# Kernel optimization log

Hardware: AMD Instinct MI355X
Metric: run time of the kernel (lower is better)

Reference implementation:

```python
import jax, jax.numpy as jnp
import numpy as np

B, S, HID = 2, 2048, 1024
NH, DK, DV = 4, 256, 256   # head_k_dim = head_v_dim = 1024 / 4
KSZ = 4                    # conv_size
EPS = 1e-5


def causal_conv1d(x, w):
    # x: [B, S, C] channels-last, w: [C, K] depthwise kernel (torch [C,1,K] squeezed)
    K = w.shape[1]
    Sn = x.shape[1]
    xp = jnp.pad(x, ((0, 0), (K - 1, 0), (0, 0)))
    # cross-correlation with left padding K-1 -> causal: out[t] = sum_j w[:,j] * x[t-(K-1)+j]
    out = xp[:, 0:Sn, :] * w[:, 0]
    for j in range(1, K):
        out = out + xp[:, j:j + Sn, :] * w[:, j]
    return out


def l2norm(x, eps=1e-6):
    return x * jax.lax.rsqrt(jnp.sum(x * x, axis=-1, keepdims=True) + eps)


def rms_norm(x, w, eps=EPS):
    return x * jax.lax.rsqrt(jnp.mean(x * x, axis=-1, keepdims=True) + eps) * w


def delta_rule(q, k, v, beta):
    # q,k: [B,S,H,dk]; v: [B,S,H,dv]; beta: [B,S,H]
    Bn, Sn, Hn, dk = q.shape
    dv = v.shape[-1]
    N = Bn * Hn
    qs = jnp.moveaxis(q, 1, 0).reshape(Sn, N, dk)
    ks = jnp.moveaxis(k, 1, 0).reshape(Sn, N, dk)
    vs = jnp.moveaxis(v, 1, 0).reshape(Sn, N, dv)
    bs = jnp.moveaxis(beta, 1, 0).reshape(Sn, N)

    S0 = jnp.zeros((N, dk, dv), q.dtype)

    def step(St, inp):
        qt, kt, vt, bt = inp
        kS = jnp.einsum('nk,nkv->nv', kt, St)              # k^T S
        St = St + jnp.einsum('nk,nv->nkv', kt, bt[:, None] * (vt - kS))
        ot = jnp.einsum('nk,nkv->nv', qt, St)
        return St, ot

    _, o = jax.lax.scan(step, S0, (qs, ks, vs, bs))        # o: [S, N, dv]
    o = o.reshape(Sn, Bn, Hn, dv)
    return jnp.moveaxis(o, 0, 1)                            # [B,S,H,dv]


def setup_inputs() -> dict:
    key = jax.random.key(0)
    ks = jax.random.split(key, 10)
    w_scale = 2.0 ** (-2.5) * np.sqrt(6.0 / (HID + HID))   # xavier_uniform with gain 2^-2.5
    u = lambda k, shp, s: jax.random.uniform(k, shp, jnp.float32, -s, s)
    return {
        'hidden_states': jax.random.normal(ks[0], (B, S, HID), jnp.float32),
        'Wq': u(ks[1], (HID, NH * DK), w_scale),
        'Wk': u(ks[2], (HID, NH * DK), w_scale),
        'Wv': u(ks[3], (HID, NH * DV), w_scale),
        'Wb': u(ks[4], (HID, NH), w_scale),
        'conv_q': jax.random.normal(ks[5], (NH * DK, KSZ), jnp.float32) * 0.2,
        'conv_k': jax.random.normal(ks[6], (NH * DK, KSZ), jnp.float32) * 0.2,
        'conv_v': jax.random.normal(ks[7], (NH * DV, KSZ), jnp.float32) * 0.2,
        'norm_w': jnp.ones((DV,), jnp.float32),
        'Wo': u(ks[8], (NH * DV, HID), w_scale),
    }


def reference(hidden_states, Wq, Wk, Wv, Wb, conv_q, conv_k, conv_v, norm_w, Wo):
    q = hidden_states @ Wq                                  # [B,S,key_dim]
    k = hidden_states @ Wk
    v = hidden_states @ Wv
    q = causal_conv1d(q, conv_q)
    k = causal_conv1d(k, conv_k)
    v = causal_conv1d(v, conv_v)
    q = jax.nn.silu(q).reshape(B, S, NH, DK)
    k = jax.nn.silu(k).reshape(B, S, NH, DK)
    v = jax.nn.silu(v).reshape(B, S, NH, DV)
    beta = jax.nn.sigmoid(hidden_states @ Wb)               # [B,S,H]
    q = l2norm(q)
    k = l2norm(k)
    o = delta_rule(q, k, v, beta)                           # [B,S,H,dv]
    o = rms_norm(o, norm_w)
    o = o.reshape(B, S, NH * DV) @ Wo                       # [B,S,HID]
    return o
```

## Files before the change

kernel.cpp:

```cpp
#include <hip/hip_runtime.h>
#include <math.h>

#define BB   2
#define SS   2048
#define HIDD 1024
#define ROWS 4096
#define NCH  32
#define CH   64

typedef unsigned short u16t;
typedef unsigned int   u32t;

typedef __attribute__((ext_vector_type(8))) short bf16x8;
typedef __attribute__((ext_vector_type(4))) float f32x4;

__device__ __forceinline__ float bf2f(u16t u) { return __uint_as_float(((u32t)u) << 16); }
__device__ __forceinline__ u16t f2bf(float f) {
    u32t b = __float_as_uint(f);
    return (u16t)((b + 0x7FFFu + ((b >> 16) & 1u)) >> 16);
}
__device__ __forceinline__ float lo_bf(u32t u) { return __uint_as_float(u << 16); }
__device__ __forceinline__ float hi_bf(u32t u) { return __uint_as_float(u & 0xFFFF0000u); }

__device__ __forceinline__ float waveReduceSum(float v) {
#pragma unroll
    for (int m = 1; m < 64; m <<= 1) v += __shfl_xor(v, m, 64);
    return v;
}

__device__ __forceinline__ void gload16(const void* g, void* l) {
    __builtin_amdgcn_global_load_lds(
        (const __attribute__((address_space(1))) unsigned int*)g,
        (__attribute__((address_space(3))) unsigned int*)l, 16, 0, 0);
}

#define MFMA(a, b, c) __builtin_amdgcn_mfma_f32_16x16x32_bf16(a, b, c, 0, 0, 0)

__global__ __launch_bounds__(256) void f2bf_kernel(const float* __restrict__ in,
                                                   u16t* __restrict__ out) {
    const size_t idx = ((size_t)blockIdx.x * 256 + threadIdx.x) * 8;
    float4 a = *(const float4*)&in[idx];
    float4 b = *(const float4*)&in[idx + 4];
    ushort4 o1, o2;
    o1.x = f2bf(a.x); o1.y = f2bf(a.y); o1.z = f2bf(a.z); o1.w = f2bf(a.w);
    o2.x = f2bf(b.x); o2.y = f2bf(b.y); o2.z = f2bf(b.z); o2.w = f2bf(b.w);
    *(ushort4*)&out[idx] = o1;
    *(ushort4*)&out[idx + 4] = o2;
}

__global__ __launch_bounds__(256) void transpose_w4(const float* __restrict__ W0,
                                                    const float* __restrict__ W1,
                                                    const float* __restrict__ W2,
                                                    const float* __restrict__ W3,
                                                    u16t* __restrict__ T0,
                                                    u16t* __restrict__ T1,
                                                    u16t* __restrict__ T2,
                                                    u16t* __restrict__ T3) {
    __shared__ u16t tile[64][65];
    const int z = blockIdx.z;
    const float* W = (z == 0) ? W0 : (z == 1) ? W1 : (z == 2) ? W2 : W3;
    u16t* WT = (z == 0) ? T0 : (z == 1) ? T1 : (z == 2) ? T2 : T3;
    const int t = threadIdx.x;
    const int r0 = blockIdx.y * 64, c0 = blockIdx.x * 64;
    const int lr = t >> 2, lc4 = (t & 3) * 16;
#pragma unroll
    for (int m = 0; m < 4; ++m) {
        float4 v = *(const float4*)&W[(size_t)(r0 + lr) * 1024 + c0 + lc4 + m * 4];
        tile[lr][lc4 + m * 4 + 0] = f2bf(v.x);
        tile[lr][lc4 + m * 4 + 1] = f2bf(v.y);
        tile[lr][lc4 + m * 4 + 2] = f2bf(v.z);
        tile[lr][lc4 + m * 4 + 3] = f2bf(v.w);
    }
    __syncthreads();
#pragma unroll
    for (int m = 0; m < 16; ++m)
        WT[(size_t)(c0 + lr) * 1024 + r0 + lc4 + m] = tile[lc4 + m][lr];
}

__global__ __launch_bounds__(256) void gemm_mfma(const u16t* __restrict__ A,
                                                 const u16t* __restrict__ BT,
                                                 float* __restrict__ Cf,
                                                 u16t* __restrict__ Cb, int obf,
                                                 int M, int N, int K,
                                                 size_t bStrideP, size_t cStrideP,
                                                 int CX) {
    __shared__ u16t As[128 * 64];
    __shared__ u16t Bs[128 * 64];
    const int t = threadIdx.x, l = t & 63, w = t >> 6;
    const int wr = w >> 1, wc = w & 1;

    const int lin = blockIdx.y * gridDim.x + blockIdx.x;
    const int xcd = lin & 7, idx = lin >> 3;
    const int Wc = gridDim.x / CX;
    const int Hc = (gridDim.y * CX) >> 3;
    const int colB = (xcd % CX) * Wc + idx % Wc;
    const int rowB = (xcd / CX) * Hc + idx / Wc;

    const int rowBase = rowB * 128, colBase = colB * 128;
    const int l15 = l & 15, g4 = l >> 4;

    const int bplane = colBase >> 10;
    const int bcol = colBase & 1023;

    const int srow = l >> 3;
    const int sj = (l & 7) ^ srow;
    const u16t* aSrc = A + (size_t)(rowBase + srow) * K + sj * 8;
    const u16t* bSrc = BT + (size_t)bplane * bStrideP + (size_t)(bcol + srow) * K + sj * 8;

    f32x4 acc[4][4];
#pragma unroll
    for (int i = 0; i < 4; ++i)
#pragma unroll
        for (int j = 0; j < 4; ++j) acc[i][j] = (f32x4){0.f, 0.f, 0.f, 0.f};

    for (int k0 = 0; k0 < K; k0 += 64) {
#pragma unroll
        for (int i = 0; i < 4; ++i) {
            const int rb = (i * 4 + w) * 8;
            gload16(aSrc + (size_t)rb * K + k0, &As[rb * 64]);
            gload16(bSrc + (size_t)rb * K + k0, &Bs[rb * 64]);
        }
        __syncthreads();
#pragma unroll
        for (int kh = 0; kh < 2; ++kh) {
            bf16x8 aF[4], bF[4];
#pragma unroll
            for (int mi = 0; mi < 4; ++mi) {
                const int row = wr * 64 + mi * 16 + l15;
                const int phys = (kh * 4 + g4) ^ (row & 7);
                aF[mi] = *(const bf16x8*)&As[row * 64 + phys * 8];
            }
#pragma unroll
            for (int ni = 0; ni < 4; ++ni) {
                const int row = wc * 64 + ni * 16 + l15;
                const int phys = (kh * 4 + g4) ^ (row & 7);
                bF[ni] = *(const bf16x8*)&Bs[row * 64 + phys * 8];
            }
#pragma unroll
            for (int mi = 0; mi < 4; ++mi)
#pragma unroll
                for (int ni = 0; ni < 4; ++ni)
                    acc[mi][ni] = MFMA(aF[mi], bF[ni], acc[mi][ni]);
        }
        __syncthreads();
    }
#pragma unroll
    for (int mi = 0; mi < 4; ++mi)
#pragma unroll
        for (int ni = 0; ni < 4; ++ni)
#pragma unroll
            for (int rg = 0; rg < 4; ++rg) {
                const int row = rowBase + wr * 64 + mi * 16 + g4 * 4 + rg;
                const int col = colBase + wc * 64 + ni * 16 + l15;
                const int plane = col >> 10, cc = col & 1023;
                const float v = acc[mi][ni][rg];
                if (obf) Cb[(size_t)plane * cStrideP + (size_t)row * 1024 + cc] = f2bf(v);
                else     Cf[(size_t)plane * cStrideP + (size_t)row * 1024 + cc] = v;
            }
}

__global__ __launch_bounds__(256) void beta_kernel(const float* __restrict__ X,
                                                   const float* __restrict__ Wb,
                                                   float* __restrict__ beta) {
    const int gw   = (blockIdx.x * blockDim.x + threadIdx.x) >> 6;
    const int lane = threadIdx.x & 63;
    if (gw >= ROWS) return;
    const float* x = X + (size_t)gw * HIDD;
    float a0 = 0.f, a1 = 0.f, a2 = 0.f, a3 = 0.f;
#pragma unroll
    for (int i = 0; i < 4; ++i) {
        const int k = lane * 16 + i * 4;
        float4 xv = *(const float4*)&x[k];
        float4 w0 = *(const float4*)&Wb[(size_t)(k + 0) * 4];
        float4 w1 = *(const float4*)&Wb[(size_t)(k + 1) * 4];
        float4 w2 = *(const float4*)&Wb[(size_t)(k + 2) * 4];
        float4 w3 = *(const float4*)&Wb[(size_t)(k + 3) * 4];
        a0 += xv.x * w0.x + xv.y * w1.x + xv.z * w2.x + xv.w * w3.x;
        a1 += xv.x * w0.y + xv.y * w1.y + xv.z * w2.y + xv.w * w3.y;
        a2 += xv.x * w0.z + xv.y * w1.z + xv.z * w2.z + xv.w * w3.z;
        a3 += xv.x * w0.w + xv.y * w1.w + xv.z * w2.w + xv.w * w3.w;
    }
    a0 = waveReduceSum(a0); a1 = waveReduceSum(a1);
    a2 = waveReduceSum(a2); a3 = waveReduceSum(a3);
    if (lane == 0) {
        float4 o = make_float4(1.f / (1.f + expf(-a0)), 1.f / (1.f + expf(-a1)),
                               1.f / (1.f + expf(-a2)), 1.f / (1.f + expf(-a3)));
        *(float4*)&beta[(size_t)gw * 4] = o;
    }
}

__global__ __launch_bounds__(256) void conv_qv(const u16t* __restrict__ inQ,
                                               const float* __restrict__ wQ,
                                               u16t* __restrict__ outQ,
                                               const u16t* __restrict__ inV,
                                               const float* __restrict__ wV,
                                               u16t* __restrict__ outV) {
    const int isQ = (blockIdx.y == 0);
    const u16t* in = isQ ? inQ : inV;
    const float* w = isQ ? wQ : wV;
    u16t* out      = isQ ? outQ : outV;
    const int doL2 = isQ;

    const int gw   = (blockIdx.x * blockDim.x + threadIdx.x) >> 6;
    const int lane = threadIdx.x & 63;
    const int r = gw >> 2;
    const int h = gw & 3;
    const int b = r >> 11;
    const int s = r & 2047;
    const int c4 = h * 256 + lane * 4;

    const float4 wr0 = *(const float4*)&w[(size_t)(c4 + 0) * 4];
    const float4 wr1 = *(const float4*)&w[(size_t)(c4 + 1) * 4];
    const float4 wr2 = *(const float4*)&w[(size_t)(c4 + 2) * 4];
    const float4 wr3 = *(const float4*)&w[(size_t)(c4 + 3) * 4];

    const size_t rowB = (size_t)(b << 11);
    float x0[4] = {0, 0, 0, 0}, x1[4] = {0, 0, 0, 0}, x2[4] = {0, 0, 0, 0}, x3[4];
    ushort4 u;
    if (s >= 3) { u = *(const ushort4*)&in[(rowB + s - 3) * HIDD + c4];
        x0[0] = bf2f(u.x); x0[1] = bf2f(u.y); x0[2] = bf2f(u.z); x0[3] = bf2f(u.w); }
    if (s >= 2) { u = *(const ushort4*)&in[(rowB + s - 2) * HIDD + c4];
        x1[0] = bf2f(u.x); x1[1] = bf2f(u.y); x1[2] = bf2f(u.z); x1[3] = bf2f(u.w); }
    if (s >= 1) { u = *(const ushort4*)&in[(rowB + s - 1) * HIDD + c4];
        x2[0] = bf2f(u.x); x2[1] = bf2f(u.y); x2[2] = bf2f(u.z); x2[3] = bf2f(u.w); }
    u = *(const ushort4*)&in[(rowB + s) * HIDD + c4];
    x3[0] = bf2f(u.x); x3[1] = bf2f(u.y); x3[2] = bf2f(u.z); x3[3] = bf2f(u.w);

    float y0 = wr0.x * x0[0] + wr0.y * x1[0] + wr0.z * x2[0] + wr0.w * x3[0];
    float y1 = wr1.x * x0[1] + wr1.y * x1[1] + wr1.z * x2[1] + wr1.w * x3[1];
    float y2 = wr2.x * x0[2] + wr2.y * x1[2] + wr2.z * x2[2] + wr2.w * x3[2];
    float y3 = wr3.x * x0[3] + wr3.y * x1[3] + wr3.z * x2[3] + wr3.w * x3[3];

    y0 = y0 / (1.f + expf(-y0)); y1 = y1 / (1.f + expf(-y1));
    y2 = y2 / (1.f + expf(-y2)); y3 = y3 / (1.f + expf(-y3));

    if (doL2) {
        float ss = y0 * y0 + y1 * y1 + y2 * y2 + y3 * y3;
        ss = waveReduceSum(ss);
        float sc = rsqrtf(ss + 1e-6f);
        y0 *= sc; y1 *= sc; y2 *= sc; y3 *= sc;
    }
    ushort4 o;
    o.x = f2bf(y0); o.y = f2bf(y1); o.z = f2bf(y2); o.w = f2bf(y3);
    *(ushort4*)&out[(size_t)r * HIDD + c4] = o;
}

__global__ __launch_bounds__(256) void conv_k_chunk(const u16t* __restrict__ pre,
                                                    const float* __restrict__ w,
                                                    u16t* __restrict__ rowout,
                                                    u16t* __restrict__ trout) {
    const int t = threadIdx.x;
    const int bh = blockIdx.x >> 5, c = blockIdx.x & 31;
    const int b = bh >> 2, h = bh & 3;
    const int i = t >> 2, g = t & 3;
    const int s = c * 64 + i;
    const size_t row = (size_t)b * 2048 + s;
    const int ch0 = h * 256 + g * 64;
    const int cloc = g * 64;
    float y[64];
#pragma unroll
    for (int m = 0; m < 8; ++m) {
        const int cm = ch0 + m * 8;
        uint4 x3 = *(const uint4*)&pre[row * 1024 + cm];
        uint4 x2 = (s >= 1) ? *(const uint4*)&pre[(row - 1) * 1024 + cm] : make_uint4(0, 0, 0, 0);
        uint4 x1 = (s >= 2) ? *(const uint4*)&pre[(row - 2) * 1024 + cm] : make_uint4(0, 0, 0, 0);
        uint4 x0 = (s >= 3) ? *(const uint4*)&pre[(row - 3) * 1024 + cm] : make_uint4(0, 0, 0, 0);
        u32t c0[4] = {x0.x, x0.y, x0.z, x0.w};
        u32t c1[4] = {x1.x, x1.y, x1.z, x1.w};
        u32t c2[4] = {x2.x, x2.y, x2.z, x2.w};
        u32t c3[4] = {x3.x, x3.y, x3.z, x3.w};
#pragma unroll
        for (int p = 0; p < 4; ++p) {
            const int ch = m * 8 + p * 2;
            float4 wA = *(const float4*)&w[(size_t)(ch0 + ch) * 4];
            float4 wB = *(const float4*)&w[(size_t)(ch0 + ch + 1) * 4];
            float ya = wA.x * lo_bf(c0[p]) + wA.y * lo_bf(c1[p]) + wA.z * lo_bf(c2[p]) + wA.w * lo_bf(c3[p]);
            float yb = wB.x * hi_bf(c0[p]) + wB.y * hi_bf(c1[p]) + wB.z * hi_bf(c2[p]) + wB.w * hi_bf(c3[p]);
            ya = ya / (1.f + expf(-ya));
            yb = yb / (1.f + expf(-yb));
            y[ch] = ya; y[ch + 1] = yb;
        }
    }
    float ss = 0.f;
#pragma unroll
    for (int e = 0; e < 64; ++e) ss += y[e] * y[e];
    ss += __shfl_xor(ss, 1);
    ss += __shfl_xor(ss, 2);
    const float sc = rsqrtf(ss + 1e-6f);
#pragma unroll
    for (int m = 0; m < 8; ++m) {
        uint4 o;
        u32t* op = (u32t*)&o;
#pragma unroll
        for (int p = 0; p < 4; ++p) {
            u16t a = f2bf(y[m * 8 + p * 2] * sc);
            u16t bb2 = f2bf(y[m * 8 + p * 2 + 1] * sc);
            op[p] = (u32t)a | ((u32t)bb2 << 16);
        }
        *(uint4*)&rowout[row * 1024 + ch0 + m * 8] = o;
    }
#pragma unroll
    for (int e = 0; e < 64; ++e)
        trout[((size_t)bh * 256 + cloc + e) * 2048 + s] = f2bf(y[e] * sc);
}

__global__ __launch_bounds__(256) void prep_kernel(const u16t* __restrict__ qcb,
                                                   const u16t* __restrict__ kcb,
                                                   const float* __restrict__ beta,
                                                   u16t* __restrict__ Tghi,
                                                   u16t* __restrict__ Tglo,
                                                   u16t* __restrict__ Agb) {
    __shared__ float KT[256][68];
    __shared__ float QT[256][68];
    __shared__ float Af[64][68];
    const int t = threadIdx.x;
    const int bhc = blockIdx.x;
    const int bh = bhc >> 5, c = bhc & 31;
    const int b = bh >> 2, h = bh & 3;
    const int tb = b * SS + c * CH;

    {
        const int i = t & 63, rb = t >> 6;
        const u16t* kg = kcb + (size_t)(tb + i) * HIDD + h * 256 + rb * 64;
        const u16t* qg = qcb + (size_t)(tb + i) * HIDD + h * 256 + rb * 64;
#pragma unroll
        for (int m = 0; m < 8; ++m) {
            uint4 kv = ((const uint4*)kg)[m];
            uint4 qv = ((const uint4*)qg)[m];
            u32t kw[4] = {kv.x, kv.y, kv.z, kv.w};
            u32t qw[4] = {qv.x, qv.y, qv.z, qv.w};
#pragma unroll
            for (int n = 0; n < 4; ++n) {
                int rr = rb * 64 + m * 8 + n * 2;
                KT[rr][i]     = lo_bf(kw[n]);
                KT[rr + 1][i] = hi_bf(kw[n]);
                QT[rr][i]     = lo_bf(qw[n]);
                QT[rr + 1][i] = hi_bf(qw[n]);
            }
        }
    }
    __syncthreads();

    const int it = t & 63, jb = t >> 6;
    float kk[16], qk[16];
#pragma unroll
    for (int m = 0; m < 16; ++m) { kk[m] = 0.f; qk[m] = 0.f; }
#pragma unroll 2
    for (int r = 0; r < 256; ++r) {
        float ki = KT[r][it];
        float qi = QT[r][it];
        float4 ka = *(const float4*)&KT[r][jb * 16 + 0];
        float4 kb = *(const float4*)&KT[r][jb * 16 + 4];
        float4 kc = *(const float4*)&KT[r][jb * 16 + 8];
        float4 kd = *(const float4*)&KT[r][jb * 16 + 12];
        float kj[16] = {ka.x, ka.y, ka.z, ka.w, kb.x, kb.y, kb.z, kb.w,
                        kc.x, kc.y, kc.z, kc.w, kd.x, kd.y, kd.z, kd.w};
#pragma unroll
        for (int m = 0; m < 16; ++m) { kk[m] += ki * kj[m]; qk[m] += qi * kj[m]; }
    }

    const float bta = beta[(size_t)(tb + it) * 4 + h];
    u16t* ag = Agb + (size_t)bhc * 4096 + (size_t)it * 64 + jb * 16;
#pragma unroll
    for (int m = 0; m < 16; ++m) {
        int j = jb * 16 + m;
        Af[it][j] = (j < it) ? bta * kk[m] : 0.f;
    }
#pragma unroll
    for (int m4 = 0; m4 < 4; ++m4) {
        ushort4 o;
        o.x = f2bf((jb * 16 + m4 * 4 + 0 <= it) ? qk[m4 * 4 + 0] : 0.f);
        o.y = f2bf((jb * 16 + m4 * 4 + 1 <= it) ? qk[m4 * 4 + 1] : 0.f);
        o.z = f2bf((jb * 16 + m4 * 4 + 2 <= it) ? qk[m4 * 4 + 2] : 0.f);
        o.w = f2bf((jb * 16 + m4 * 4 + 3 <= it) ? qk[m4 * 4 + 3] : 0.f);
        *(ushort4*)&ag[m4 * 4] = o;
    }
    __syncthreads();

    if (t < 64) {
        const int ccol = t;
        float tc[64];
#pragma unroll
        for (int j = 0; j < 64; ++j) tc[j] = (j == ccol) ? 1.f : 0.f;
#pragma unroll
        for (int i = 1; i < 64; ++i) {
            float a = 0.f;
#pragma unroll
            for (int j = 0; j < i; ++j) a += Af[i][j] * tc[j];
            tc[i] -= a;
        }
        u16t* th = Tghi + (size_t)bhc * 4096;
        u16t* tl = Tglo + (size_t)bhc * 4096;
#pragma unroll
        for (int i = 0; i < 64; ++i) {
            u16t hi = f2bf(tc[i]);
            th[i * 64 + ccol] = hi;
            tl[i * 64 + ccol] = f2bf(tc[i] - bf2f(hi));
        }
    }
}

__global__ __launch_bounds__(256, 1) void scan_mfma(const u16t* __restrict__ qcb,
                                                    const u16t* __restrict__ kcb,
                                                    const u16t* __restrict__ ktr,
                                                    const u16t* __restrict__ vcb,
                                                    const float* __restrict__ beta,
                                                    const u16t* __restrict__ TghiG,
                                                    const u16t* __restrict__ TgloG,
                                                    const u16t* __restrict__ AgbG,
                                                    u16t* __restrict__ o_raw) {
    __shared__ u16t Shi[16 * 256];
    __shared__ u16t Slo[16 * 256];
    __shared__ u16t Rhi[16 * 64];
    __shared__ u16t Rlo[16 * 64];
    __shared__ u16t Uhi[16 * 64];
    __shared__ u16t Ulo[16 * 64];

    const int t = threadIdx.x, l = t & 63, w = t >> 6;
    const int bh = blockIdx.x & 7, vt = blockIdx.x >> 3;
    const int b = bh >> 2, h = bh & 3;
    const int vcol0 = vt * 16;
    const int vlow = l & 15, g4 = l >> 4;

    for (int i = t; i < 16 * 256; i += 256) { Shi[i] = 0; Slo[i] = 0; }
    f32x4 sf[4];
#pragma unroll
    for (int q = 0; q < 4; ++q) sf[q] = (f32x4){0.f, 0.f, 0.f, 0.f};

    bf16x8 kf[8], qf[8], tfh[2], tfl[2], af[2], kcf[8];
    u16t vfb[4];
    float bta[4];

    auto loadKQ = [&](int c) {
        const size_t rb = (size_t)(b * 2048 + c * 64 + 16 * w + vlow) * 1024 + h * 256 + g4 * 8;
#pragma unroll
        for (int ks = 0; ks < 8; ++ks) {
            kf[ks] = *(const bf16x8*)(kcb + rb + ks * 32);
            qf[ks] = *(const bf16x8*)(qcb + rb + ks * 32);
        }
    };
    auto loadVB = [&](int c) {
        const int r0 = b * 2048 + c * 64 + 16 * w + 4 * g4;
#pragma unroll
        for (int rg = 0; rg < 4; ++rg) {
            vfb[rg] = vcb[(size_t)(r0 + rg) * 1024 + h * 256 + vcol0 + vlow];
            bta[rg] = beta[(size_t)(r0 + rg) * 4 + h];
        }
    };
    auto loadT = [&](int c) {
        const size_t tb2 = (size_t)(bh * 32 + c) * 4096 + (size_t)(16 * w + vlow) * 64 + g4 * 8;
        tfh[0] = *(const bf16x8*)(TghiG + tb2);
        tfh[1] = *(const bf16x8*)(TghiG + tb2 + 32);
        tfl[0] = *(const bf16x8*)(TgloG + tb2);
        tfl[1] = *(const bf16x8*)(TgloG + tb2 + 32);
    };
    auto loadA = [&](int c) {
        const size_t tb2 = (size_t)(bh * 32 + c) * 4096 + (size_t)(16 * w + vlow) * 64 + g4 * 8;
        af[0] = *(const bf16x8*)(AgbG + tb2);
        af[1] = *(const bf16x8*)(AgbG + tb2 + 32);
    };
    auto loadKC = [&](int c) {
        const size_t cb2 = ((size_t)bh * 256 + 64 * w + vlow) * 2048 + c * 64 + g4 * 8;
#pragma unroll
        for (int q2 = 0; q2 < 4; ++q2) {
            kcf[q2 * 2 + 0] = *(const bf16x8*)(ktr + cb2 + (size_t)(16 * q2) * 2048);
            kcf[q2 * 2 + 1] = *(const bf16x8*)(ktr + cb2 + (size_t)(16 * q2) * 2048 + 32);
        }
    };

    loadKQ(0); loadVB(0); loadT(0); loadA(0); loadKC(0);
    __syncthreads();

    for (int c = 0; c < NCH; ++c) {
        const int cn = (c + 1 < NCH) ? c + 1 : c;
        const int trow0 = b * 2048 + c * 64;

        f32x4 Wacc = (f32x4){0.f, 0.f, 0.f, 0.f};
        f32x4 O1   = (f32x4){0.f, 0.f, 0.f, 0.f};
#pragma unroll
        for (int ks = 0; ks < 8; ++ks) {
            const int pb = (((ks * 4 + g4) ^ (vlow & 7)) << 3);
            bf16x8 bH = *(const bf16x8*)&Shi[vlow * 256 + pb];
            bf16x8 bL = *(const bf16x8*)&Slo[vlow * 256 + pb];
            Wacc = MFMA(kf[ks], bH, Wacc); Wacc = MFMA(kf[ks], bL, Wacc);
            O1   = MFMA(qf[ks], bH, O1);   O1   = MFMA(qf[ks], bL, O1);
        }
        {
            const int tslot = 2 * w + (g4 >> 1);
            const int base = vlow * 64 + ((tslot ^ (vlow & 7)) << 3) + ((g4 & 1) << 2);
            u16t rh[4], rl[4];
#pragma unroll
            for (int rg = 0; rg < 4; ++rg) {
                float rv = bta[rg] * (bf2f(vfb[rg]) - Wacc[rg]);
                rh[rg] = f2bf(rv);
                rl[rg] = f2bf(rv - bf2f(rh[rg]));
            }
            uint2 ph, pl;
            ph.x = (u32t)rh[0] | ((u32t)rh[1] << 16); ph.y = (u32t)rh[2] | ((u32t)rh[3] << 16);
            pl.x = (u32t)rl[0] | ((u32t)rl[1] << 16); pl.y = (u32t)rl[2] | ((u32t)rl[3] << 16);
            *(uint2*)&Rhi[base] = ph;
            *(uint2*)&Rlo[base] = pl;
        }
        loadKQ(cn);
        loadVB(cn);
        __syncthreads();

        f32x4 Uacc = (f32x4){0.f, 0.f, 0.f, 0.f};
#pragma unroll
        for (int ks = 0; ks < 2; ++ks) {
            const int pb = (((ks * 4 + g4) ^ (vlow & 7)) << 3);
            bf16x8 bH = *(const bf16x8*)&Rhi[vlow * 64 + pb];
            bf16x8 bL = *(const bf16x8*)&Rlo[vlow * 64 + pb];
            Uacc = MFMA(tfh[ks], bH, Uacc);
            Uacc = MFMA(tfh[ks], bL, Uacc);
            Uacc = MFMA(tfl[ks], bH, Uacc);
        }
        {
            const int tslot = 2 * w + (g4 >> 1);
            const int base = vlow * 64 + ((tslot ^ (vlow & 7)) << 3) + ((g4 & 1) << 2);
            u16t uh[4], ul[4];
#pragma unroll
            for (int rg = 0; rg < 4; ++rg) {
                uh[rg] = f2bf(Uacc[rg]);
                ul[rg] = f2bf(Uacc[rg] - bf2f(uh[rg]));
            }
            uint2 ph, pl;
            ph.x = (u32t)uh[0] | ((u32t)uh[1] << 16); ph.y = (u32t)uh[2] | ((u32t)uh[3] << 16);
            pl.x = (u32t)ul[0] | ((u32t)ul[1] << 16); pl.y = (u32t)ul[2] | ((u32t)ul[3] << 16);
            *(uint2*)&Uhi[base] = ph;
            *(uint2*)&Ulo[base] = pl;
        }
        loadT(cn);
        __syncthreads();

        bf16x8 uhf[2], ulf[2];
#pragma unroll
        for (int ks = 0; ks < 2; ++ks) {
            const int pb = (((ks * 4 + g4) ^ (vlow & 7)) << 3);
            uhf[ks] = *(const bf16x8*)&Uhi[vlow * 64 + pb];
            ulf[ks] = *(const bf16x8*)&Ulo[vlow * 64 + pb];
        }
        f32x4 Oacc = O1;
#pragma unroll
        for (int ks = 0; ks < 2; ++ks) {
            Oacc = MFMA(af[ks], uhf[ks], Oacc);
            Oacc = MFMA(af[ks], ulf[ks], Oacc);
        }
#pragma unroll
        for (int rg = 0; rg < 4; ++rg)
            o_raw[(size_t)(trow0 + 16 * w + 4 * g4 + rg) * 1024 + h * 256 + vcol0 + vlow] = f2bf(Oacc[rg]);
        loadA(cn);

#pragma unroll
        for (int q = 0; q < 4; ++q) {
#pragma unroll
            for (int ks = 0; ks < 2; ++ks) {
                sf[q] = MFMA(kcf[q * 2 + ks], uhf[ks], sf[q]);
                sf[q] = MFMA(kcf[q * 2 + ks], ulf[ks], sf[q]);
            }
        }
        loadKC(cn);

#pragma unroll
        for (int q = 0; q < 4; ++q) {
            u16t sh[4], sl[4];
#pragma unroll
            for (int rg = 0; rg < 4; ++rg) {
                u16t hi = f2bf(sf[q][rg]);
                sh[rg] = hi;
                sl[rg] = f2bf(sf[q][rg] - bf2f(hi));
            }
            const int rslot = 8 * w + 2 * q + (g4 >> 1);
            const int base = vlow * 256 + ((rslot ^ (vlow & 7)) << 3) + ((g4 & 1) << 2);
            uint2 ph, pl;
            ph.x = (u32t)sh[0] | ((u32t)sh[1] << 16); ph.y = (u32t)sh[2] | ((u32t)sh[3] << 16);
            pl.x = (u32t)sl[0] | ((u32t)sl[1] << 16); pl.y = (u32t)sl[2] | ((u32t)sl[3] << 16);
            *(uint2*)&Shi[base] = ph;
            *(uint2*)&Slo[base] = pl;
        }
        __syncthreads();
    }
}

__global__ __launch_bounds__(256) void rms_kernel(const u16t* __restrict__ in,
                                                  const float* __restrict__ w,
                                                  u16t* __restrict__ out) {
    const int gw   = (blockIdx.x * blockDim.x + threadIdx.x) >> 6;
    const int lane = threadIdx.x & 63;
    const int r = gw >> 2;
    const int h = gw & 3;
    const size_t base = (size_t)r * HIDD + h * 256 + lane * 4;
    ushort4 xv = *(const ushort4*)&in[base];
    float x0 = bf2f(xv.x), x1 = bf2f(xv.y), x2 = bf2f(xv.z), x3 = bf2f(xv.w);
    float ss = x0 * x0 + x1 * x1 + x2 * x2 + x3 * x3;
    ss = waveReduceSum(ss);
    const float sc = rsqrtf(ss * (1.0f / 256.0f) + 1e-5f);
    float4 wv = *(const float4*)&w[lane * 4];
    ushort4 o;
    o.x = f2bf(x0 * sc * wv.x); o.y = f2bf(x1 * sc * wv.y);
    o.z = f2bf(x2 * sc * wv.z); o.w = f2bf(x3 * sc * wv.w);
    *(ushort4*)&out[base] = o;
}

extern "C" void kernel_launch(void* const* d_in, const int* in_sizes, int n_in,
                              void* d_out, int out_size, void* d_ws, size_t ws_size,
                              hipStream_t stream) {
    const float* X      = (const float*)d_in[0];
    const float* Wq     = (const float*)d_in[1];
    const float* Wk     = (const float*)d_in[2];
    const float* Wv     = (const float*)d_in[3];
    const float* Wb     = (const float*)d_in[4];
    const float* conv_q = (const float*)d_in[5];
    const float* conv_k = (const float*)d_in[6];
    const float* conv_v = (const float*)d_in[7];
    const float* norm_w = (const float*)d_in[8];
    const float* Wo     = (const float*)d_in[9];
    float* out = (float*)d_out;

    char* W8 = (char*)d_ws;
    const size_t MB = 1u << 20;
    u16t* Xbf   = (u16t*)(W8 + 0 * MB);
    u16t* o_raw = Xbf;
    u16t* qpre  = (u16t*)(W8 + 8 * MB);
    u16t* o_nrm = qpre;
    u16t* kpre  = (u16t*)(W8 + 16 * MB);
    u16t* Tghi  = (u16t*)(W8 + 16 * MB);
    u16t* Tglo  = (u16t*)(W8 + 18 * MB);
    u16t* Agb   = (u16t*)(W8 + 20 * MB);
    u16t* vpre  = (u16t*)(W8 + 24 * MB);
    u16t* ktr   = (u16t*)(W8 + 24 * MB);
    u16t* WqT   = (u16t*)(W8 + 32 * MB);
    u16t* qcb   = (u16t*)(W8 + 32 * MB);
    u16t* WkT   = (u16t*)(W8 + 40 * MB);
    u16t* kcb   = (u16t*)(W8 + 40 * MB);
    u16t* WvT   = (u16t*)(W8 + 48 * MB);
    u16t* vcb   = (u16t*)(W8 + 48 * MB);
    u16t* WoT   = (u16t*)(W8 + 56 * MB);
    float* betab = (float*)(W8 + 58 * MB);

    const size_t PL = 4194304;

    f2bf_kernel<<<2048, 256, 0, stream>>>(X, Xbf);
    transpose_w4<<<dim3(16, 16, 4), 256, 0, stream>>>(Wq, Wk, Wv, Wo, WqT, WkT, WvT, WoT);

    gemm_mfma<<<dim3(24, 32), 256, 0, stream>>>(Xbf, WqT, nullptr, qpre, 1,
                                                ROWS, 3072, HIDD, PL, PL, 2);
    beta_kernel<<<ROWS / 4, 256, 0, stream>>>(X, Wb, betab);

    conv_qv<<<dim3(ROWS, 2), 256, 0, stream>>>(qpre, conv_q, qcb, vpre, conv_v, vcb);
    conv_k_chunk<<<256, 256, 0, stream>>>(kpre, conv_k, kcb, ktr);

    prep_kernel<<<256, 256, 0, stream>>>(qcb, kcb, betab, Tghi, Tglo, Agb);
    scan_mfma<<<128, 256, 0, stream>>>(qcb, kcb, ktr, vcb, betab, Tghi, Tglo, Agb, o_raw);

    rms_kernel<<<ROWS, 256, 0, stream>>>(o_raw, norm_w, o_nrm);
    gemm_mfma<<<dim3(8, 32), 256, 0, stream>>>(o_nrm, WoT, out, nullptr, 0,
                                               ROWS, HIDD, HIDD, 0, 0, 1);
}
```

Before: 285.9 us.

## Process four value-column tiles per scan block to reuse K/Q/T/A fragments

Each scan block now handles 64 value columns (four 16-wide tiles) instead of 16, so the per-chunk K, Q, T, A and transposed-K fragments loaded from global memory are reused across four state slices. The grid shrinks from 128 to 32 blocks, and shared memory and accumulator registers grow fourfold. The goal is to cut redundant global loads of the shared operands, at the cost of parallelism (only 32 CUs busy on a chip with many more) and higher register pressure.

```diff
diff --git a/kernel.cpp b/kernel.cpp
--- a/kernel.cpp
+++ b/kernel.cpp
@@ -409,26 +409,29 @@
                                                     const u16t* __restrict__ TgloG,
                                                     const u16t* __restrict__ AgbG,
                                                     u16t* __restrict__ o_raw) {
-    __shared__ u16t Shi[16 * 256];
-    __shared__ u16t Slo[16 * 256];
-    __shared__ u16t Rhi[16 * 64];
-    __shared__ u16t Rlo[16 * 64];
-    __shared__ u16t Uhi[16 * 64];
-    __shared__ u16t Ulo[16 * 64];
+    __shared__ u16t Shi[4][16 * 256];
+    __shared__ u16t Slo[4][16 * 256];
+    __shared__ u16t Rhi[4][16 * 64];
+    __shared__ u16t Rlo[4][16 * 64];
+    __shared__ u16t Uhi[4][16 * 64];
+    __shared__ u16t Ulo[4][16 * 64];
 
     const int t = threadIdx.x, l = t & 63, w = t >> 6;
-    const int bh = blockIdx.x & 7, vt = blockIdx.x >> 3;
+    const int bh = blockIdx.x & 7, vq = blockIdx.x >> 3;
     const int b = bh >> 2, h = bh & 3;
-    const int vcol0 = vt * 16;
+    const int vbase = vq * 64;
     const int vlow = l & 15, g4 = l >> 4;
 
-    for (int i = t; i < 16 * 256; i += 256) { Shi[i] = 0; Slo[i] = 0; }
-    f32x4 sf[4];
-#pragma unroll
-    for (int q = 0; q < 4; ++q) sf[q] = (f32x4){0.f, 0.f, 0.f, 0.f};
+    for (int i = t; i < 4 * 16 * 256; i += 256) { (&Shi[0][0])[i] = 0; (&Slo[0][0])[i] = 0; }
+
+    f32x4 sf[4][4];
+#pragma unroll
+    for (int p = 0; p < 4; ++p)
+#pragma unroll
+        for (int q = 0; q < 4; ++q) sf[p][q] = (f32x4){0.f, 0.f, 0.f, 0.f};
 
     bf16x8 kf[8], qf[8], tfh[2], tfl[2], af[2], kcf[8];
-    u16t vfb[4];
+    u16t vfb[4][4];
     float bta[4];
 
     auto loadKQ = [&](int c) {
@@ -443,8 +446,10 @@
         const int r0 = b * 2048 + c * 64 + 16 * w + 4 * g4;
 #pragma unroll
         for (int rg = 0; rg < 4; ++rg) {
-            vfb[rg] = vcb[(size_t)(r0 + rg) * 1024 + h * 256 + vcol0 + vlow];
             bta[rg] = beta[(size_t)(r0 + rg) * 4 + h];
+#pragma unroll
+            for (int p = 0; p < 4; ++p)
+                vfb[p][rg] = vcb[(size_t)(r0 + rg) * 1024 + h * 256 + vbase + p * 16 + vlow];
         }
     };
     auto loadT = [&](int c) {
@@ -471,113 +476,125 @@
     loadKQ(0); loadVB(0); loadT(0); loadA(0); loadKC(0);
     __syncthreads();
 
+    const int tslot = 2 * w + (g4 >> 1);
+    const int rubase = vlow * 64 + ((tslot ^ (vlow & 7)) << 3) + ((g4 & 1) << 2);
+
     for (int c = 0; c < NCH; ++c) {
         const int cn = (c + 1 < NCH) ? c + 1 : c;
         const int trow0 = b * 2048 + c * 64;
 
-        f32x4 Wacc = (f32x4){0.f, 0.f, 0.f, 0.f};
-        f32x4 O1   = (f32x4){0.f, 0.f, 0.f, 0.f};
+        f32x4 Wacc[4], O1[4];
+#pragma unroll
+        for (int p = 0; p < 4; ++p) { Wacc[p] = (f32x4){0,0,0,0}; O1[p] = (f32x4){0,0,0,0}; }
 #pragma unroll
         for (int ks = 0; ks < 8; ++ks) {
             const int pb = (((ks * 4 + g4) ^ (vlow & 7)) << 3);
-            bf16x8 bH = *(const bf16x8*)&Shi[vlow * 256 + pb];
-            bf16x8 bL = *(const bf16x8*)&Slo[vlow * 256 + pb];
-            Wacc = MFMA(kf[ks], bH, Wacc); Wacc = MFMA(kf[ks], bL, Wacc);
-            O1   = MFMA(qf[ks], bH, O1);   O1   = MFMA(qf[ks], bL, O1);
-        }
-        {
-            const int tslot = 2 * w + (g4 >> 1);
-            const int base = vlow * 64 + ((tslot ^ (vlow & 7)) << 3) + ((g4 & 1) << 2);
+#pragma unroll
+            for (int p = 0; p < 4; ++p) {
+                bf16x8 bH = *(const bf16x8*)&Shi[p][vlow * 256 + pb];
+                bf16x8 bL = *(const bf16x8*)&Slo[p][vlow * 256 + pb];
+                Wacc[p] = MFMA(kf[ks], bH, Wacc[p]); Wacc[p] = MFMA(kf[ks], bL, Wacc[p]);
+                O1[p]   = MFMA(qf[ks], bH, O1[p]);   O1[p]   = MFMA(qf[ks], bL, O1[p]);
+            }
+        }
+#pragma unroll
+        for (int p = 0; p < 4; ++p) {
             u16t rh[4], rl[4];
 #pragma unroll
             for (int rg = 0; rg < 4; ++rg) {
-                float rv = bta[rg] * (bf2f(vfb[rg]) - Wacc[rg]);
+                float rv = bta[rg] * (bf2f(vfb[p][rg]) - Wacc[p][rg]);
                 rh[rg] = f2bf(rv);
                 rl[rg] = f2bf(rv - bf2f(rh[rg]));
             }
             uint2 ph, pl;
             ph.x = (u32t)rh[0] | ((u32t)rh[1] << 16); ph.y = (u32t)rh[2] | ((u32t)rh[3] << 16);
             pl.x = (u32t)rl[0] | ((u32t)rl[1] << 16); pl.y = (u32t)rl[2] | ((u32t)rl[3] << 16);
-            *(uint2*)&Rhi[base] = ph;
-            *(uint2*)&Rlo[base] = pl;
+            *(uint2*)&Rhi[p][rubase] = ph;
+            *(uint2*)&Rlo[p][rubase] = pl;
         }
         loadKQ(cn);
         loadVB(cn);
         __syncthreads();
 
-        f32x4 Uacc = (f32x4){0.f, 0.f, 0.f, 0.f};
+        f32x4 Uacc[4];
+#pragma unroll
+        for (int p = 0; p < 4; ++p) Uacc[p] = (f32x4){0,0,0,0};
 #pragma unroll
         for (int ks = 0; ks < 2; ++ks) {
             const int pb = (((ks * 4 + g4) ^ (vlow & 7)) << 3);
-            bf16x8 bH = *(const bf16x8*)&Rhi[vlow * 64 + pb];
-            bf16x8 bL = *(const bf16x8*)&Rlo[vlow * 64 + pb];
-            Uacc = MFMA(tfh[ks], bH, Uacc);
-            Uacc = MFMA(tfh[ks], bL, Uacc);
-            Uacc = MFMA(tfl[ks], bH, Uacc);
-        }
-        {
-            const int tslot = 2 * w + (g4 >> 1);
-            const int base = vlow * 64 + ((tslot ^ (vlow & 7)) << 3) + ((g4 & 1) << 2);
+#pragma unroll
+            for (int p = 0; p < 4; ++p) {
+                bf16x8 bH = *(const bf16x8*)&Rhi[p][vlow * 64 + pb];
+                bf16x8 bL = *(const bf16x8*)&Rlo[p][vlow * 64 + pb];
+                Uacc[p] = MFMA(tfh[ks], bH, Uacc[p]);
+                Uacc[p] = MFMA(tfh[ks], bL, Uacc[p]);
+                Uacc[p] = MFMA(tfl[ks], bH, Uacc[p]);
+            }
+        }
+#pragma unroll
+        for (int p = 0; p < 4; ++p) {
             u16t uh[4], ul[4];
 #pragma unroll
             for (int rg = 0; rg < 4; ++rg) {
-                uh[rg] = f2bf(Uacc[rg]);
-                ul[rg] = f2bf(Uacc[rg] - bf2f(uh[rg]));
+                uh[rg] = f2bf(Uacc[p][rg]);
+                ul[rg] = f2bf(Uacc[p][rg] - bf2f(uh[rg]));
             }
             uint2 ph, pl;
             ph.x = (u32t)uh[0] | ((u32t)uh[1] << 16); ph.y = (u32t)uh[2] | ((u32t)uh[3] << 16);
             pl.x = (u32t)ul[0] | ((u32t)ul[1] << 16); pl.y = (u32t)ul[2] | ((u32t)ul[3] << 16);
-            *(uint2*)&Uhi[base] = ph;
-            *(uint2*)&Ulo[base] = pl;
+            *(uint2*)&Uhi[p][rubase] = ph;
+            *(uint2*)&Ulo[p][rubase] = pl;
         }
         loadT(cn);
         __syncthreads();
 
-        bf16x8 uhf[2], ulf[2];
-#pragma unroll
-        for (int ks = 0; ks < 2; ++ks) {
-            const int pb = (((ks * 4 + g4) ^ (vlow & 7)) << 3);
-            uhf[ks] = *(const bf16x8*)&Uhi[vlow * 64 + pb];
-            ulf[ks] = *(const bf16x8*)&Ulo[vlow * 64 + pb];
-        }
-        f32x4 Oacc = O1;
-#pragma unroll
-        for (int ks = 0; ks < 2; ++ks) {
-            Oacc = MFMA(af[ks], uhf[ks], Oacc);
-            Oacc = MFMA(af[ks], ulf[ks], Oacc);
-        }
-#pragma unroll
-        for (int rg = 0; rg < 4; ++rg)
-            o_raw[(size_t)(trow0 + 16 * w + 4 * g4 + rg) * 1024 + h * 256 + vcol0 + vlow] = f2bf(Oacc[rg]);
+#pragma unroll
+        for (int p = 0; p < 4; ++p) {
+            bf16x8 uhf[2], ulf[2];
+#pragma unroll
+            for (int ks = 0; ks < 2; ++ks) {
+                const int pb = (((ks * 4 + g4) ^ (vlow & 7)) << 3);
+                uhf[ks] = *(const bf16x8*)&Uhi[p][vlow * 64 + pb];
+                ulf[ks] = *(const bf16x8*)&Ulo[p][vlow * 64 + pb];
+            }
+            f32x4 Oacc = O1[p];
+#pragma unroll
+            for (int ks = 0; ks < 2; ++ks) {
+                Oacc = MFMA(af[ks], uhf[ks], Oacc);
+                Oacc = MFMA(af[ks], ulf[ks], Oacc);
+            }
+#pragma unroll
+            for (int rg = 0; rg < 4; ++rg)
+                o_raw[(size_t)(trow0 + 16 * w + 4 * g4 + rg) * 1024 + h * 256 + vbase + p * 16 + vlow] = f2bf(Oacc[rg]);
+
+#pragma unroll
+            for (int q = 0; q < 4; ++q) {
+#pragma unroll
+                for (int ks = 0; ks < 2; ++ks) {
+                    sf[p][q] = MFMA(kcf[q * 2 + ks], uhf[ks], sf[p][q]);
+                    sf[p][q] = MFMA(kcf[q * 2 + ks], ulf[ks], sf[p][q]);
+                }
+            }
+#pragma unroll
+            for (int q = 0; q < 4; ++q) {
+                u16t sh[4], sl[4];
+#pragma unroll
+                for (int rg = 0; rg < 4; ++rg) {
+                    u16t hi = f2bf(sf[p][q][rg]);
+                    sh[rg] = hi;
+                    sl[rg] = f2bf(sf[p][q][rg] - bf2f(hi));
+                }
+                const int rslot = 8 * w + 2 * q + (g4 >> 1);
+                const int base = vlow * 256 + ((rslot ^ (vlow & 7)) << 3) + ((g4 & 1) << 2);
+                uint2 ph, pl;
+                ph.x = (u32t)sh[0] | ((u32t)sh[1] << 16); ph.y = (u32t)sh[2] | ((u32t)sh[3] << 16);
+                pl.x = (u32t)sl[0] | ((u32t)sl[1] << 16); pl.y = (u32t)sl[2] | ((u32t)sl[3] << 16);
+                *(uint2*)&Shi[p][base] = ph;
+                *(uint2*)&Slo[p][base] = pl;
+            }
+        }
         loadA(cn);
-
-#pragma unroll
-        for (int q = 0; q < 4; ++q) {
-#pragma unroll
-            for (int ks = 0; ks < 2; ++ks) {
-                sf[q] = MFMA(kcf[q * 2 + ks], uhf[ks], sf[q]);
-                sf[q] = MFMA(kcf[q * 2 + ks], ulf[ks], sf[q]);
-            }
-        }
         loadKC(cn);
-
-#pragma unroll
-        for (int q = 0; q < 4; ++q) {
-            u16t sh[4], sl[4];
-#pragma unroll
-            for (int rg = 0; rg < 4; ++rg) {
-                u16t hi = f2bf(sf[q][rg]);
-                sh[rg] = hi;
-                sl[rg] = f2bf(sf[q][rg] - bf2f(hi));
-            }
-            const int rslot = 8 * w + 2 * q + (g4 >> 1);
-            const int base = vlow * 256 + ((rslot ^ (vlow & 7)) << 3) + ((g4 & 1) << 2);
-            uint2 ph, pl;
-            ph.x = (u32t)sh[0] | ((u32t)sh[1] << 16); ph.y = (u32t)sh[2] | ((u32t)sh[3] << 16);
-            pl.x = (u32t)sl[0] | ((u32t)sl[1] << 16); pl.y = (u32t)sl[2] | ((u32t)sl[3] << 16);
-            *(uint2*)&Shi[base] = ph;
-            *(uint2*)&Slo[base] = pl;
-        }
         __syncthreads();
     }
 }
@@ -651,7 +668,7 @@
     conv_k_chunk<<<256, 256, 0, stream>>>(kpre, conv_k, kcb, ktr);
 
     prep_kernel<<<256, 256, 0, stream>>>(qcb, kcb, betab, Tghi, Tglo, Agb);
-    scan_mfma<<<128, 256, 0, stream>>>(qcb, kcb, ktr, vcb, betab, Tghi, Tglo, Agb, o_raw);
+    scan_mfma<<<32, 256, 0, stream>>>(qcb, kcb, ktr, vcb, betab, Tghi, Tglo, Agb, o_raw);
 
     rms_kernel<<<ROWS, 256, 0, stream>>>(o_raw, norm_w, o_nrm);
     gemm_mfma<<<dim3(8, 32), 256, 0, stream>>>(o_nrm, WoT, out, nullptr, 0,
```

After: 395.0 us. 38.1% more time.

## Merge chunk pairs into 128-step macro-chunks in delta-rule scan

Applied to the files above, without the earlier changes.

Adds a prep2 kernel that precomputes the cross-chunk coupling block T21 = -T22·(beta·K2K1ᵀ)·T11 and the Q2K1ᵀ block, so the scan can process two 64-step chunks per iteration as one 128-step macro-chunk with 512 threads. This halves the number of serial iterations and barriers in the recurrent scan, which is latency-bound with only 128 blocks. In exchange it adds an extra kernel launch, more global reads of the T/A matrices, wave-divergent work between the lower and upper halves, and some extra precision error from composing the T blocks in fp32 and splitting them into bf16 hi/lo pairs.

```diff
diff --git a/kernel.cpp b/kernel.cpp
--- a/kernel.cpp
+++ b/kernel.cpp
@@ -7,6 +7,7 @@
 #define ROWS 4096
 #define NCH  32
 #define CH   64
+#define NMC  16
 
 typedef unsigned short u16t;
 typedef unsigned int   u32t;
@@ -400,7 +401,102 @@
     }
 }
 
-__global__ __launch_bounds__(256, 1) void scan_mfma(const u16t* __restrict__ qcb,
+__global__ __launch_bounds__(256) void prep2_kernel(const u16t* __restrict__ qcb,
+                                                    const u16t* __restrict__ kcb,
+                                                    const float* __restrict__ beta,
+                                                    const u16t* __restrict__ Tghi,
+                                                    const u16t* __restrict__ Tglo,
+                                                    u16t* __restrict__ T21hi,
+                                                    u16t* __restrict__ T21lo,
+                                                    u16t* __restrict__ A21g) {
+    __shared__ float Gs[64][68];
+    __shared__ float T11f[64][68];
+    __shared__ float T22f[64][68];
+    __shared__ float Pf[64][68];
+
+    const int t = threadIdx.x, l = t & 63, w = t >> 6;
+    const int bhmc = blockIdx.x;
+    const int bh = bhmc >> 4, mc = bhmc & 15;
+    const int b = bh >> 2, h = bh & 3;
+    const int t1 = b * SS + mc * 128;
+    const int t2 = t1 + 64;
+    const int vlow = l & 15, g4 = l >> 4;
+
+    bf16x8 k2f[8], q2f[8];
+    {
+        const size_t rb = (size_t)(t2 + 16 * w + vlow) * 1024 + h * 256 + g4 * 8;
+#pragma unroll
+        for (int ks = 0; ks < 8; ++ks) {
+            k2f[ks] = *(const bf16x8*)(kcb + rb + ks * 32);
+            q2f[ks] = *(const bf16x8*)(qcb + rb + ks * 32);
+        }
+    }
+    float bta2[4];
+#pragma unroll
+    for (int rg = 0; rg < 4; ++rg)
+        bta2[rg] = beta[(size_t)(t2 + 16 * w + 4 * g4 + rg) * 4 + h];
+
+#pragma unroll
+    for (int jt = 0; jt < 4; ++jt) {
+        bf16x8 k1f[8];
+        const size_t rb1 = (size_t)(t1 + 16 * jt + vlow) * 1024 + h * 256 + g4 * 8;
+#pragma unroll
+        for (int ks = 0; ks < 8; ++ks)
+            k1f[ks] = *(const bf16x8*)(kcb + rb1 + ks * 32);
+        f32x4 Gacc = (f32x4){0.f, 0.f, 0.f, 0.f};
+        f32x4 Aacc = (f32x4){0.f, 0.f, 0.f, 0.f};
+#pragma unroll
+        for (int ks = 0; ks < 8; ++ks) {
+            Gacc = MFMA(k2f[ks], k1f[ks], Gacc);
+            Aacc = MFMA(q2f[ks], k1f[ks], Aacc);
+        }
+        const int j = 16 * jt + vlow;
+#pragma unroll
+        for (int rg = 0; rg < 4; ++rg) {
+            const int i = 16 * w + 4 * g4 + rg;
+            Gs[i][j] = bta2[rg] * Gacc[rg];
+            A21g[(size_t)bhmc * 4096 + (size_t)i * 64 + j] = f2bf(Aacc[rg]);
+        }
+    }
+    {
+        const size_t b11 = (size_t)(bh * 32 + 2 * mc) * 4096;
+        const size_t b22 = (size_t)(bh * 32 + 2 * mc + 1) * 4096;
+        for (int idx = t; idx < 4096; idx += 256) {
+            const int i = idx >> 6, j = idx & 63;
+            T11f[i][j] = bf2f(Tghi[b11 + idx]) + bf2f(Tglo[b11 + idx]);
+            T22f[i][j] = bf2f(Tghi[b22 + idx]) + bf2f(Tglo[b22 + idx]);
+        }
+    }
+    __syncthreads();
+
+    {
+        const int col = t & 63, rq = t >> 6;
+        for (int ii = 0; ii < 16; ++ii) {
+            const int i = rq * 16 + ii;
+            float a = 0.f;
+#pragma unroll 8
+            for (int j = 0; j < 64; ++j) a += Gs[i][j] * T11f[j][col];
+            Pf[i][col] = a;
+        }
+    }
+    __syncthreads();
+
+    {
+        const int col = t & 63, rq = t >> 6;
+        for (int ii = 0; ii < 16; ++ii) {
+            const int i = rq * 16 + ii;
+            float a = 0.f;
+#pragma unroll 8
+            for (int j = 0; j < 64; ++j) a += T22f[i][j] * Pf[j][col];
+            a = -a;
+            const u16t hi = f2bf(a);
+            T21hi[(size_t)bhmc * 4096 + (size_t)i * 64 + col] = hi;
+            T21lo[(size_t)bhmc * 4096 + (size_t)i * 64 + col] = f2bf(a - bf2f(hi));
+        }
+    }
+}
+
+__global__ __launch_bounds__(512, 1) void scan_mfma(const u16t* __restrict__ qcb,
                                                     const u16t* __restrict__ kcb,
                                                     const u16t* __restrict__ ktr,
                                                     const u16t* __restrict__ vcb,
@@ -408,31 +504,37 @@
                                                     const u16t* __restrict__ TghiG,
                                                     const u16t* __restrict__ TgloG,
                                                     const u16t* __restrict__ AgbG,
+                                                    const u16t* __restrict__ T21hi,
+                                                    const u16t* __restrict__ T21lo,
+                                                    const u16t* __restrict__ A21g,
                                                     u16t* __restrict__ o_raw) {
     __shared__ u16t Shi[16 * 256];
     __shared__ u16t Slo[16 * 256];
-    __shared__ u16t Rhi[16 * 64];
-    __shared__ u16t Rlo[16 * 64];
-    __shared__ u16t Uhi[16 * 64];
-    __shared__ u16t Ulo[16 * 64];
+    __shared__ u16t Rhi[16 * 128];
+    __shared__ u16t Rlo[16 * 128];
+    __shared__ u16t Uhi[16 * 128];
+    __shared__ u16t Ulo[16 * 128];
 
     const int t = threadIdx.x, l = t & 63, w = t >> 6;
     const int bh = blockIdx.x & 7, vt = blockIdx.x >> 3;
     const int b = bh >> 2, h = bh & 3;
     const int vcol0 = vt * 16;
     const int vlow = l & 15, g4 = l >> 4;
-
-    for (int i = t; i < 16 * 256; i += 256) { Shi[i] = 0; Slo[i] = 0; }
-    f32x4 sf[4];
-#pragma unroll
-    for (int q = 0; q < 4; ++q) sf[q] = (f32x4){0.f, 0.f, 0.f, 0.f};
-
-    bf16x8 kf[8], qf[8], tfh[2], tfl[2], af[2], kcf[8];
+    const int sw = vlow & 7;
+    const int isHi = (w >= 4);
+    const int w4 = isHi ? (w - 4) : w;
+
+    for (int i = t; i < 16 * 256; i += 512) { Shi[i] = 0; Slo[i] = 0; }
+    f32x4 sf[2];
+    sf[0] = (f32x4){0.f, 0.f, 0.f, 0.f};
+    sf[1] = (f32x4){0.f, 0.f, 0.f, 0.f};
+
+    bf16x8 kf[8], qf[8], tfh[4], tfl[4], af[4], kcf[2][4];
     u16t vfb[4];
     float bta[4];
 
     auto loadKQ = [&](int c) {
-        const size_t rb = (size_t)(b * 2048 + c * 64 + 16 * w + vlow) * 1024 + h * 256 + g4 * 8;
+        const size_t rb = (size_t)(b * 2048 + c * 128 + 16 * w + vlow) * 1024 + h * 256 + g4 * 8;
 #pragma unroll
         for (int ks = 0; ks < 8; ++ks) {
             kf[ks] = *(const bf16x8*)(kcb + rb + ks * 32);
@@ -440,7 +542,7 @@
         }
     };
     auto loadVB = [&](int c) {
-        const int r0 = b * 2048 + c * 64 + 16 * w + 4 * g4;
+        const int r0 = b * 2048 + c * 128 + 16 * w + 4 * g4;
 #pragma unroll
         for (int rg = 0; rg < 4; ++rg) {
             vfb[rg] = vcb[(size_t)(r0 + rg) * 1024 + h * 256 + vcol0 + vlow];
@@ -448,38 +550,61 @@
         }
     };
     auto loadT = [&](int c) {
-        const size_t tb2 = (size_t)(bh * 32 + c) * 4096 + (size_t)(16 * w + vlow) * 64 + g4 * 8;
-        tfh[0] = *(const bf16x8*)(TghiG + tb2);
-        tfh[1] = *(const bf16x8*)(TghiG + tb2 + 32);
-        tfl[0] = *(const bf16x8*)(TgloG + tb2);
-        tfl[1] = *(const bf16x8*)(TgloG + tb2 + 32);
+        if (!isHi) {
+            const size_t bs = (size_t)(bh * 32 + 2 * c) * 4096 + (size_t)(16 * w + vlow) * 64 + g4 * 8;
+            tfh[0] = *(const bf16x8*)(TghiG + bs);
+            tfh[1] = *(const bf16x8*)(TghiG + bs + 32);
+            tfl[0] = *(const bf16x8*)(TgloG + bs);
+            tfl[1] = *(const bf16x8*)(TgloG + bs + 32);
+        } else {
+            const size_t b21 = (size_t)(bh * 16 + c) * 4096 + (size_t)(16 * w4 + vlow) * 64 + g4 * 8;
+            tfh[0] = *(const bf16x8*)(T21hi + b21);
+            tfh[1] = *(const bf16x8*)(T21hi + b21 + 32);
+            tfl[0] = *(const bf16x8*)(T21lo + b21);
+            tfl[1] = *(const bf16x8*)(T21lo + b21 + 32);
+            const size_t b22 = (size_t)(bh * 32 + 2 * c + 1) * 4096 + (size_t)(16 * w4 + vlow) * 64 + g4 * 8;
+            tfh[2] = *(const bf16x8*)(TghiG + b22);
+            tfh[3] = *(const bf16x8*)(TghiG + b22 + 32);
+            tfl[2] = *(const bf16x8*)(TgloG + b22);
+            tfl[3] = *(const bf16x8*)(TgloG + b22 + 32);
+        }
     };
     auto loadA = [&](int c) {
-        const size_t tb2 = (size_t)(bh * 32 + c) * 4096 + (size_t)(16 * w + vlow) * 64 + g4 * 8;
-        af[0] = *(const bf16x8*)(AgbG + tb2);
-        af[1] = *(const bf16x8*)(AgbG + tb2 + 32);
+        if (!isHi) {
+            const size_t bs = (size_t)(bh * 32 + 2 * c) * 4096 + (size_t)(16 * w + vlow) * 64 + g4 * 8;
+            af[0] = *(const bf16x8*)(AgbG + bs);
+            af[1] = *(const bf16x8*)(AgbG + bs + 32);
+        } else {
+            const size_t b21 = (size_t)(bh * 16 + c) * 4096 + (size_t)(16 * w4 + vlow) * 64 + g4 * 8;
+            af[0] = *(const bf16x8*)(A21g + b21);
+            af[1] = *(const bf16x8*)(A21g + b21 + 32);
+            const size_t b22 = (size_t)(bh * 32 + 2 * c + 1) * 4096 + (size_t)(16 * w4 + vlow) * 64 + g4 * 8;
+            af[2] = *(const bf16x8*)(AgbG + b22);
+            af[3] = *(const bf16x8*)(AgbG + b22 + 32);
+        }
     };
     auto loadKC = [&](int c) {
-        const size_t cb2 = ((size_t)bh * 256 + 64 * w + vlow) * 2048 + c * 64 + g4 * 8;
-#pragma unroll
-        for (int q2 = 0; q2 < 4; ++q2) {
-            kcf[q2 * 2 + 0] = *(const bf16x8*)(ktr + cb2 + (size_t)(16 * q2) * 2048);
-            kcf[q2 * 2 + 1] = *(const bf16x8*)(ktr + cb2 + (size_t)(16 * q2) * 2048 + 32);
+#pragma unroll
+        for (int q2 = 0; q2 < 2; ++q2) {
+            const size_t cb2 = ((size_t)bh * 256 + 32 * w + 16 * q2 + vlow) * 2048 + c * 128 + g4 * 8;
+#pragma unroll
+            for (int ks = 0; ks < 4; ++ks)
+                kcf[q2][ks] = *(const bf16x8*)(ktr + cb2 + ks * 32);
         }
     };
 
     loadKQ(0); loadVB(0); loadT(0); loadA(0); loadKC(0);
     __syncthreads();
 
-    for (int c = 0; c < NCH; ++c) {
-        const int cn = (c + 1 < NCH) ? c + 1 : c;
-        const int trow0 = b * 2048 + c * 64;
+    for (int c = 0; c < NMC; ++c) {
+        const int cn = (c + 1 < NMC) ? c + 1 : c;
+        const int trow0 = b * 2048 + c * 128;
 
         f32x4 Wacc = (f32x4){0.f, 0.f, 0.f, 0.f};
         f32x4 O1   = (f32x4){0.f, 0.f, 0.f, 0.f};
 #pragma unroll
         for (int ks = 0; ks < 8; ++ks) {
-            const int pb = (((ks * 4 + g4) ^ (vlow & 7)) << 3);
+            const int pb = (((ks * 4 + g4) ^ sw) << 3);
             bf16x8 bH = *(const bf16x8*)&Shi[vlow * 256 + pb];
             bf16x8 bL = *(const bf16x8*)&Slo[vlow * 256 + pb];
             Wacc = MFMA(kf[ks], bH, Wacc); Wacc = MFMA(kf[ks], bL, Wacc);
@@ -487,7 +612,7 @@
         }
         {
             const int tslot = 2 * w + (g4 >> 1);
-            const int base = vlow * 64 + ((tslot ^ (vlow & 7)) << 3) + ((g4 & 1) << 2);
+            const int base = vlow * 128 + ((tslot ^ sw) << 3) + ((g4 & 1) << 2);
             u16t rh[4], rl[4];
 #pragma unroll
             for (int rg = 0; rg < 4; ++rg) {
@@ -506,18 +631,18 @@
         __syncthreads();
 
         f32x4 Uacc = (f32x4){0.f, 0.f, 0.f, 0.f};
-#pragma unroll
-        for (int ks = 0; ks < 2; ++ks) {
-            const int pb = (((ks * 4 + g4) ^ (vlow & 7)) << 3);
-            bf16x8 bH = *(const bf16x8*)&Rhi[vlow * 64 + pb];
-            bf16x8 bL = *(const bf16x8*)&Rlo[vlow * 64 + pb];
+        const int NK = isHi ? 4 : 2;
+        for (int ks = 0; ks < NK; ++ks) {
+            const int pb = (((ks * 4 + g4) ^ sw) << 3);
+            bf16x8 bH = *(const bf16x8*)&Rhi[vlow * 128 + pb];
+            bf16x8 bL = *(const bf16x8*)&Rlo[vlow * 128 + pb];
             Uacc = MFMA(tfh[ks], bH, Uacc);
             Uacc = MFMA(tfh[ks], bL, Uacc);
             Uacc = MFMA(tfl[ks], bH, Uacc);
         }
         {
             const int tslot = 2 * w + (g4 >> 1);
-            const int base = vlow * 64 + ((tslot ^ (vlow & 7)) << 3) + ((g4 & 1) << 2);
+            const int base = vlow * 128 + ((tslot ^ sw) << 3) + ((g4 & 1) << 2);
             u16t uh[4], ul[4];
 #pragma unroll
             for (int rg = 0; rg < 4; ++rg) {
@@ -533,16 +658,15 @@
         loadT(cn);
         __syncthreads();
 
-        bf16x8 uhf[2], ulf[2];
-#pragma unroll
-        for (int ks = 0; ks < 2; ++ks) {
-            const int pb = (((ks * 4 + g4) ^ (vlow & 7)) << 3);
-            uhf[ks] = *(const bf16x8*)&Uhi[vlow * 64 + pb];
-            ulf[ks] = *(const bf16x8*)&Ulo[vlow * 64 + pb];
+        bf16x8 uhf[4], ulf[4];
+#pragma unroll
+        for (int ks = 0; ks < 4; ++ks) {
+            const int pb = (((ks * 4 + g4) ^ sw) << 3);
+            uhf[ks] = *(const bf16x8*)&Uhi[vlow * 128 + pb];
+            ulf[ks] = *(const bf16x8*)&Ulo[vlow * 128 + pb];
         }
         f32x4 Oacc = O1;
-#pragma unroll
-        for (int ks = 0; ks < 2; ++ks) {
+        for (int ks = 0; ks < NK; ++ks) {
             Oacc = MFMA(af[ks], uhf[ks], Oacc);
             Oacc = MFMA(af[ks], ulf[ks], Oacc);
         }
@@ -552,26 +676,26 @@
         loadA(cn);
 
 #pragma unroll
-        for (int q = 0; q < 4; ++q) {
-#pragma unroll
-            for (int ks = 0; ks < 2; ++ks) {
-                sf[q] = MFMA(kcf[q * 2 + ks], uhf[ks], sf[q]);
-                sf[q] = MFMA(kcf[q * 2 + ks], ulf[ks], sf[q]);
+        for (int q2 = 0; q2 < 2; ++q2) {
+#pragma unroll
+            for (int ks = 0; ks < 4; ++ks) {
+                sf[q2] = MFMA(kcf[q2][ks], uhf[ks], sf[q2]);
+                sf[q2] = MFMA(kcf[q2][ks], ulf[ks], sf[q2]);
             }
         }
         loadKC(cn);
 
 #pragma unroll
-        for (int q = 0; q < 4; ++q) {
+        for (int q2 = 0; q2 < 2; ++q2) {
             u16t sh[4], sl[4];
 #pragma unroll
             for (int rg = 0; rg < 4; ++rg) {
-                u16t hi = f2bf(sf[q][rg]);
+                u16t hi = f2bf(sf[q2][rg]);
                 sh[rg] = hi;
-                sl[rg] = f2bf(sf[q][rg] - bf2f(hi));
+                sl[rg] = f2bf(sf[q2][rg] - bf2f(hi));
             }
-            const int rslot = 8 * w + 2 * q + (g4 >> 1);
-            const int base = vlow * 256 + ((rslot ^ (vlow & 7)) << 3) + ((g4 & 1) << 2);
+            const int rslot = 4 * w + 2 * q2 + (g4 >> 1);
+            const int base = vlow * 256 + ((rslot ^ sw) << 3) + ((g4 & 1) << 2);
             uint2 ph, pl;
             ph.x = (u32t)sh[0] | ((u32t)sh[1] << 16); ph.y = (u32t)sh[2] | ((u32t)sh[3] << 16);
             pl.x = (u32t)sl[0] | ((u32t)sl[1] << 16); pl.y = (u32t)sl[2] | ((u32t)sl[3] << 16);
@@ -622,6 +746,9 @@
     u16t* Xbf   = (u16t*)(W8 + 0 * MB);
     u16t* o_raw = Xbf;
     u16t* qpre  = (u16t*)(W8 + 8 * MB);
+    u16t* T21hi = (u16t*)(W8 + 8 * MB);
+    u16t* T21lo = (u16t*)(W8 + 10 * MB);
+    u16t* A21g  = (u16t*)(W8 + 12 * MB);
     u16t* o_nrm = qpre;
     u16t* kpre  = (u16t*)(W8 + 16 * MB);
     u16t* Tghi  = (u16t*)(W8 + 16 * MB);
@@ -651,7 +778,9 @@
     conv_k_chunk<<<256, 256, 0, stream>>>(kpre, conv_k, kcb, ktr);
 
     prep_kernel<<<256, 256, 0, stream>>>(qcb, kcb, betab, Tghi, Tglo, Agb);
-    scan_mfma<<<128, 256, 0, stream>>>(qcb, kcb, ktr, vcb, betab, Tghi, Tglo, Agb, o_raw);
+    prep2_kernel<<<128, 256, 0, stream>>>(qcb, kcb, betab, Tghi, Tglo, T21hi, T21lo, A21g);
+    scan_mfma<<<128, 512, 0, stream>>>(qcb, kcb, ktr, vcb, betab, Tghi, Tglo, Agb,
+                                       T21hi, T21lo, A21g, o_raw);
 
     rms_kernel<<<ROWS, 256, 0, stream>>>(o_raw, norm_w, o_nrm);
     gemm_mfma<<<dim3(8, 32), 256, 0, stream>>>(o_nrm, WoT, out, nullptr, 0,
```

Measured after the change: 1.124 ms. 3.93x slower.
